# Kernel optimization log

Measured on AMD Instinct MI355X. Metric: run time of the kernel, lower is better.

The kernel has to match this reference:

```python
import jax, jax.numpy as jnp
import numpy as np

B, S, H = 1, 2048, 2048
HD, NQ, NKV = 128, 16, 4
FFH = 8192
EPS = 1e-5
ROPE_BASE = 10000.0
SOFTMAX_CAP = 50.0
CLIP_L, CLIP_R = 0.0, 1.0


def setup_inputs() -> dict:
    key = jax.random.key(0)
    ks = jax.random.split(key, 10)
    std = 0.02
    return {
        "x": jax.random.normal(ks[0], (B, S, H), dtype=jnp.float32),
        "attn_norm_w": jax.random.uniform(ks[1], (H,), minval=-1.0, maxval=1.0, dtype=jnp.float32),
        "mlp_norm_w": jax.random.uniform(ks[2], (H,), minval=-1.0, maxval=1.0, dtype=jnp.float32),
        "wq": jax.random.normal(ks[3], (H, NQ * HD), dtype=jnp.float32) * std,
        "wk": jax.random.normal(ks[4], (H, NKV * HD), dtype=jnp.float32) * std,
        "wv": jax.random.normal(ks[5], (H, NKV * HD), dtype=jnp.float32) * std,
        "wo": jax.random.normal(ks[6], (NQ * HD, H), dtype=jnp.float32) * std,
        "w_gate": jax.random.normal(ks[7], (H, FFH), dtype=jnp.float32) * std,
        "w_up": jax.random.normal(ks[8], (H, FFH), dtype=jnp.float32) * std,
        "w_down": jax.random.normal(ks[9], (FFH, H), dtype=jnp.float32) * std,
    }


def _rms_norm(x, w):
    # GroupRMSNorm with group_size=None -> whole hidden dim
    var = jnp.mean(jnp.square(x), axis=-1, keepdims=True)
    return x * jax.lax.rsqrt(var + EPS) * w


def _rope_cos_sin(seq_len, dim):
    inv_freq = 1.0 / (ROPE_BASE ** (jnp.arange(0, dim, 2, dtype=jnp.float32) / dim))
    t = jnp.arange(seq_len, dtype=jnp.float32)
    freqs = jnp.outer(t, inv_freq)                      # [S, dim/2]
    emb = jnp.concatenate([freqs, freqs], axis=-1)      # [S, dim]
    return jnp.cos(emb), jnp.sin(emb)


def _apply_rope(x, cos, sin):
    # x: [B, S, h, d]; rotate-half (LLaMA-style)
    d = x.shape[-1]
    x1, x2 = x[..., : d // 2], x[..., d // 2 :]
    rot = jnp.concatenate([-x2, x1], axis=-1)
    return x * cos[None, :, None, :] + rot * sin[None, :, None, :]


def _qk_norm(x):
    # per-head RMS norm over head_dim (qk_norm_group_size == head_dim), unit weight
    var = jnp.mean(jnp.square(x), axis=-1, keepdims=True)
    return x * jax.lax.rsqrt(var + EPS)


def reference(x, attn_norm_w, mlp_norm_w, wq, wk, wv, wo, w_gate, w_up, w_down):
    # ---- attention sub-layer ----
    h = _rms_norm(x, attn_norm_w)                                     # [B,S,H]
    q = (h @ wq).reshape(B, S, NQ, HD)
    k = (h @ wk).reshape(B, S, NKV, HD)
    v = (h @ wv).reshape(B, S, NKV, HD)

    cos, sin = _rope_cos_sin(S, HD)
    q = _apply_rope(q, cos, sin)
    k = _apply_rope(k, cos, sin)

    q = _qk_norm(q)
    k = _qk_norm(k)

    # GQA: expand kv heads to match q heads
    rep = NQ // NKV
    k = jnp.repeat(k, rep, axis=2)                                    # [B,S,NQ,HD]
    v = jnp.repeat(v, rep, axis=2)

    scale = 1.0 / jnp.sqrt(jnp.float32(HD))
    scores = jnp.einsum("bshd,bthd->bhst", q, k) * scale              # [B,NQ,S,S]
    # softmax cap: cap * tanh(s / cap)
    scores = SOFTMAX_CAP * jnp.tanh(scores / SOFTMAX_CAP)
    causal = jnp.tril(jnp.ones((S, S), dtype=bool))
    scores = jnp.where(causal[None, None], scores, -jnp.inf)
    p = jax.nn.softmax(scores, axis=-1)
    # clip range (l, r): clamp(p * (r - l) + l, 0, 1)
    p = jnp.clip(p * (CLIP_R - CLIP_L) + CLIP_L, 0.0, 1.0)
    o = jnp.einsum("bhst,bthd->bshd", p, v).reshape(B, S, NQ * HD)
    x = x + o @ wo

    # ---- MLP sub-layer (gated SiLU) ----
    h2 = _rms_norm(x, mlp_norm_w)
    mlp_out = (jax.nn.silu(h2 @ w_gate) * (h2 @ w_up)) @ w_down
    return x + mlp_out
```

## Files before the change

kernel.cpp:

```cpp
#include <hip/hip_runtime.h>

typedef __bf16 bf16;
typedef __bf16 bf16x8 __attribute__((ext_vector_type(8)));
typedef float f32x4 __attribute__((ext_vector_type(4)));

#define GLP16(gp, lp) __builtin_amdgcn_global_load_lds( \
    (const __attribute__((address_space(1))) void*)(gp), \
    (__attribute__((address_space(3))) void*)(lp), 16, 0, 0)

__device__ __forceinline__ f32x4 mfma16(bf16x8 a, bf16x8 b, f32x4 c) {
    return __builtin_amdgcn_mfma_f32_16x16x32_bf16(a, b, c, 0, 0, 0);
}

__global__ __launch_bounds__(256) void k_rmsnorm(const float* __restrict__ x,
        const float* __restrict__ w, bf16* __restrict__ out) {
    const int H = 2048;
    size_t row = blockIdx.x;
    const float* xr = x + row * H;
    int base = threadIdx.x * 8;
    float4 a = *(const float4*)(xr + base);
    float4 b = *(const float4*)(xr + base + 4);
    float ss = a.x*a.x + a.y*a.y + a.z*a.z + a.w*a.w
             + b.x*b.x + b.y*b.y + b.z*b.z + b.w*b.w;
#pragma unroll
    for (int m = 32; m > 0; m >>= 1) ss += __shfl_xor(ss, m);
    __shared__ float red[4];
    if ((threadIdx.x & 63) == 0) red[threadIdx.x >> 6] = ss;
    __syncthreads();
    float tot = red[0] + red[1] + red[2] + red[3];
    float rs = rsqrtf(tot * (1.0f / H) + 1e-5f);
    float4 wa = *(const float4*)(w + base);
    float4 wb = *(const float4*)(w + base + 4);
    bf16x8 ov;
    ov[0] = (bf16)(a.x * rs * wa.x); ov[1] = (bf16)(a.y * rs * wa.y);
    ov[2] = (bf16)(a.z * rs * wa.z); ov[3] = (bf16)(a.w * rs * wa.w);
    ov[4] = (bf16)(b.x * rs * wb.x); ov[5] = (bf16)(b.y * rs * wb.y);
    ov[6] = (bf16)(b.z * rs * wb.z); ov[7] = (bf16)(b.w * rs * wb.w);
    *(bf16x8*)(out + row * H + base) = ov;
}

__global__ __launch_bounds__(256) void k_convT(const float* __restrict__ W,
        bf16* __restrict__ Wt, int K, int N) {
    __shared__ float t[32][33];
    int k0 = blockIdx.x * 32, n0 = blockIdx.y * 32;
    int tx = threadIdx.x, ty = threadIdx.y;
#pragma unroll
    for (int i = 0; i < 4; i++)
        t[ty + i * 8][tx] = W[(size_t)(k0 + ty + i * 8) * N + n0 + tx];
    __syncthreads();
#pragma unroll
    for (int i = 0; i < 4; i++)
        Wt[(size_t)(n0 + ty + i * 8) * K + k0 + tx] = (bf16)t[tx][ty + i * 8];
}

__global__ __launch_bounds__(256) void k_transpose(const bf16* __restrict__ in,
        bf16* __restrict__ out, int R, int C) {
    __shared__ bf16 t[32][33];
    int r0 = blockIdx.x * 32, c0 = blockIdx.y * 32;
    int tx = threadIdx.x & 31, ty = threadIdx.x >> 5;
#pragma unroll
    for (int i = 0; i < 4; i++)
        t[ty + i * 8][tx] = in[(size_t)(r0 + ty + i * 8) * C + c0 + tx];
    __syncthreads();
#pragma unroll
    for (int i = 0; i < 4; i++)
        out[(size_t)(c0 + ty + i * 8) * R + r0 + tx] = t[tx][ty + i * 8];
}

template<int EPI>
__global__ __launch_bounds__(512) void k_gemm2(const bf16* __restrict__ A,
        const bf16* __restrict__ Bt, void* __restrict__ outp,
        const void* __restrict__ aux, int M, int N, int K, int ksplit) {
    extern __shared__ char lds[];
    const int tid = threadIdx.x, wave = tid >> 6, lane = tid & 63;
    const int lr = lane & 15, kg = lane >> 4;
    const int wm = wave >> 1, wn = wave & 1;
    const int bn = blockIdx.x, bm = blockIdx.y, split = blockIdx.z;
    const int row0 = bm * 256, col0 = bn * 128;
    const int kbeg = split * ksplit;
    const int NT = ksplit >> 6;
    const size_t K2 = (size_t)K * 2;

    size_t offA[4];
#pragma unroll
    for (int s = 0; s < 4; s++) {
        int d = s * 8192 + tid * 16;
        int ps = d ^ (((d >> 7) & 7) << 4);
        offA[s] = (size_t)(ps >> 7) * K2 + (ps & 127);
    }
    const char* Abase = (const char*)(A + (size_t)row0 * K + kbeg);
    const char* Bbase = (const char*)(Bt + (size_t)col0 * K + kbeg);

    auto stageA = [&](int t) {
        const char* src = Abase + (size_t)t * 128;
        char* dst = lds + ((t & 1) * 32768) + wave * 1024;
#pragma unroll
        for (int s = 0; s < 4; s++)
            GLP16(src + offA[s], dst + s * 8192);
    };
    auto stageB = [&](int t, int bidx) {
        const char* src = Bbase + (size_t)t * 128;
        char* dst = lds + 65536 + bidx * 16384 + wave * 1024;
#pragma unroll
        for (int s = 0; s < 2; s++)
            GLP16(src + offA[s], dst + s * 8192);
    };

    f32x4 acc[4][4];
#pragma unroll
    for (int m = 0; m < 4; m++)
#pragma unroll
        for (int n = 0; n < 4; n++) acc[m][n] = (f32x4){0, 0, 0, 0};

    stageA(0); stageB(0, 0); stageB(1, 1);
    asm volatile("s_waitcnt vmcnt(2)" ::: "memory");
    __builtin_amdgcn_s_barrier();
    __builtin_amdgcn_sched_barrier(0);
    asm volatile("" ::: "memory");

    const int xorm = (lr & 7) << 4;
    int bcur = 0;
    for (int t = 0; t < NT; ++t) {
        if (t + 1 < NT) stageA(t + 1);
        int bnx = bcur + 2; if (bnx >= 3) bnx -= 3;
        if (t + 2 < NT) stageB(t + 2, bnx);
        const char* As_ = lds + ((t & 1) * 32768);
        const char* Bs_ = lds + 65536 + bcur * 16384;
#pragma unroll
        for (int h = 0; h < 2; ++h) {
            const int inner = (h * 64 + kg * 16) ^ xorm;
            bf16x8 av[4], bv[4];
#pragma unroll
            for (int m = 0; m < 4; m++)
                av[m] = *(const bf16x8*)(As_ + (wm * 64 + m * 16 + lr) * 128 + inner);
#pragma unroll
            for (int n = 0; n < 4; n++)
                bv[n] = *(const bf16x8*)(Bs_ + (wn * 64 + n * 16 + lr) * 128 + inner);
#pragma unroll
            for (int m = 0; m < 4; m++)
#pragma unroll
                for (int n = 0; n < 4; n++)
                    acc[m][n] = mfma16(av[m], bv[n], acc[m][n]);
        }
        if (t + 1 < NT) {
            if (t + 2 < NT) asm volatile("s_waitcnt vmcnt(2)" ::: "memory");
            else            asm volatile("s_waitcnt vmcnt(0)" ::: "memory");
            __builtin_amdgcn_s_barrier();
            __builtin_amdgcn_sched_barrier(0);
            asm volatile("" ::: "memory");
        }
        bcur++; if (bcur == 3) bcur = 0;
    }

#pragma unroll
    for (int m = 0; m < 4; m++)
#pragma unroll
        for (int n = 0; n < 4; n++)
#pragma unroll
            for (int r = 0; r < 4; r++) {
                size_t row = row0 + wm * 64 + m * 16 + kg * 4 + r;
                size_t col = col0 + wn * 64 + n * 16 + lr;
                size_t idx = row * N + col;
                float vv = acc[m][n][r];
                if (EPI == 0) {
                    ((bf16*)outp)[idx] = (bf16)vv;
                } else if (EPI == 2) {
                    float g = (float)((const bf16*)aux)[idx];
                    float sg = g / (1.0f + __expf(-g));
                    ((bf16*)outp)[idx] = (bf16)(sg * vv);
                } else if (EPI == 3) {
                    ((float*)outp)[(size_t)split * M * N + idx] = vv;
                } else {
                    bf16* base = (bf16*)outp;
                    if (col < 2048)
                        base[row * 2048 + col] = (bf16)vv;
                    else if (col < 2560)
                        base[4194304 + row * 512 + (col - 2048)] = (bf16)vv;
                    else
                        base[5242880 + row * 512 + (col - 2560)] = (bf16)vv;
                }
            }
}

__global__ __launch_bounds__(256) void k_reduce(const float* __restrict__ parts,
        const float* __restrict__ resid, float* __restrict__ out,
        int ns, size_t n4) {
    size_t i = (size_t)blockIdx.x * 256 + threadIdx.x;
    if (i >= n4) return;
    float4 acc = ((const float4*)resid)[i];
    for (int s = 0; s < ns; s++) {
        float4 p = ((const float4*)(parts + (size_t)s * n4 * 4))[i];
        acc.x += p.x; acc.y += p.y; acc.z += p.z; acc.w += p.w;
    }
    ((float4*)out)[i] = acc;
}

__global__ __launch_bounds__(256) void k_reduce_rms(const float* __restrict__ parts,
        const float* __restrict__ resid, const float* __restrict__ w,
        float* __restrict__ x2, bf16* __restrict__ hb, int ns) {
    const int H = 2048;
    size_t row = blockIdx.x;
    int base = threadIdx.x * 8;
    const float* rr = resid + row * H + base;
    float4 a = *(const float4*)rr;
    float4 b = *(const float4*)(rr + 4);
    for (int s = 0; s < ns; s++) {
        const float* pp = parts + (size_t)s * H * 2048 + row * H + base;
        float4 pa = *(const float4*)pp;
        float4 pb = *(const float4*)(pp + 4);
        a.x += pa.x; a.y += pa.y; a.z += pa.z; a.w += pa.w;
        b.x += pb.x; b.y += pb.y; b.z += pb.z; b.w += pb.w;
    }
    *(float4*)(x2 + row * H + base) = a;
    *(float4*)(x2 + row * H + base + 4) = b;
    float ss = a.x*a.x + a.y*a.y + a.z*a.z + a.w*a.w
             + b.x*b.x + b.y*b.y + b.z*b.z + b.w*b.w;
#pragma unroll
    for (int m = 32; m > 0; m >>= 1) ss += __shfl_xor(ss, m);
    __shared__ float red[4];
    if ((threadIdx.x & 63) == 0) red[threadIdx.x >> 6] = ss;
    __syncthreads();
    float tot = red[0] + red[1] + red[2] + red[3];
    float rs = rsqrtf(tot * (1.0f / H) + 1e-5f);
    float4 wa = *(const float4*)(w + base);
    float4 wb = *(const float4*)(w + base + 4);
    bf16x8 ov;
    ov[0] = (bf16)(a.x * rs * wa.x); ov[1] = (bf16)(a.y * rs * wa.y);
    ov[2] = (bf16)(a.z * rs * wa.z); ov[3] = (bf16)(a.w * rs * wa.w);
    ov[4] = (bf16)(b.x * rs * wb.x); ov[5] = (bf16)(b.y * rs * wb.y);
    ov[6] = (bf16)(b.z * rs * wb.z); ov[7] = (bf16)(b.w * rs * wb.w);
    *(bf16x8*)(hb + row * H + base) = ov;
}

__global__ __launch_bounds__(64) void k_rope(bf16* __restrict__ q,
        bf16* __restrict__ k) {
    int s = blockIdx.x, hid = blockIdx.y, lane = threadIdx.x;
    bf16* p;
    if (hid < 16) p = q + (size_t)s * 2048 + hid * 128;
    else          p = k + (size_t)s * 512 + (hid - 16) * 128;
    float x1 = (float)p[lane], x2 = (float)p[lane + 64];
    float f = exp2f((float)lane * -0.2076205059304601f);
    float sn, cs;
    sincosf((float)s * f, &sn, &cs);
    float o1 = x1 * cs - x2 * sn;
    float o2 = x2 * cs + x1 * sn;
    float ss = o1 * o1 + o2 * o2;
#pragma unroll
    for (int m = 32; m > 0; m >>= 1) ss += __shfl_xor(ss, m);
    float rs = rsqrtf(ss * (1.0f / 128.0f) + 1e-5f);
    p[lane] = (bf16)(o1 * rs);
    p[lane + 64] = (bf16)(o2 * rs);
}

__global__ __launch_bounds__(256) void k_attn(const bf16* __restrict__ qg,
        const bf16* __restrict__ kgl, const bf16* __restrict__ vtg,
        bf16* __restrict__ og) {
    extern __shared__ char alds[];
    int pi = blockIdx.x, h = blockIdx.y, kvh = h >> 2;
    int tid = threadIdx.x, wave = tid >> 6, lane = tid & 63;
    int lr = lane & 15, kgrp = lane >> 4;

    int rowQ[4], colQ[4], rowV[4], colV[4];
#pragma unroll
    for (int j = 0; j < 4; j++) {
        int p = j * 4096 + wave * 1024 + lane * 16;
        int ps = p ^ (((p >> 8) & 7) << 4);
        rowQ[j] = ps >> 8; colQ[j] = ps & 255;
        int pv = p ^ (((p >> 7) & 7) << 4);
        rowV[j] = pv >> 7; colV[j] = pv & 127;
    }

    const float C1 = 0.08838834764831845f / 50.0f;
    const float L2E50 = 72.13475204444817f;

#pragma unroll 1
    for (int half = 0; half < 2; ++half) {
        int qt = half ? (31 - pi) : pi;
        int nt = qt + 1;

#pragma unroll
        for (int j = 0; j < 4; j++)
            GLP16((const char*)qg + (size_t)(qt * 64 + rowQ[j]) * 4096 + h * 256 + colQ[j],
                  alds + j * 4096 + wave * 1024);
        for (int t = 0; t < 2 && t < nt; t++) {
#pragma unroll
            for (int j = 0; j < 4; j++)
                GLP16((const char*)kgl + (size_t)(t * 64 + rowQ[j]) * 1024 + kvh * 256 + colQ[j],
                      alds + 16384 + t * 16384 + j * 4096 + wave * 1024);
#pragma unroll
            for (int j = 0; j < 4; j++)
                GLP16((const char*)vtg + (size_t)(kvh * 128 + rowV[j]) * 4096 + t * 128 + colV[j],
                      alds + 49152 + t * 16384 + j * 4096 + wave * 1024);
        }
        if (nt > 1) asm volatile("s_waitcnt vmcnt(8)" ::: "memory");
        else        asm volatile("s_waitcnt vmcnt(0)" ::: "memory");
        __builtin_amdgcn_s_barrier();

        bf16x8 qf[4];
#pragma unroll
        for (int c = 0; c < 4; c++) {
            int b = (wave * 16 + lr) * 256 + c * 64 + kgrp * 16;
            qf[c] = *(const bf16x8*)(alds + (b ^ (((b >> 8) & 7) << 4)));
        }
        f32x4 accO[8];
#pragma unroll
        for (int n = 0; n < 8; n++) accO[n] = (f32x4){0, 0, 0, 0};
        float lsum[4] = {0, 0, 0, 0};
        int qrow = qt * 64 + wave * 16 + kgrp * 4;

        for (int kt = 0; kt < nt; kt++) {
            int buf = kt & 1;
            const char* Kb = alds + 16384 + buf * 16384;
            const char* Vb = alds + 49152 + buf * 16384;
            char* Pb = alds + 81920;
#pragma unroll
            for (int j = 0; j < 4; j++) {
                f32x4 s = {0, 0, 0, 0};
#pragma unroll
                for (int c = 0; c < 4; c++) {
                    int b = (j * 16 + lr) * 256 + c * 64 + kgrp * 16;
                    bf16x8 kf = *(const bf16x8*)(Kb + (b ^ (((b >> 8) & 7) << 4)));
                    s = mfma16(qf[c], kf, s);
                }
                int key = kt * 64 + j * 16 + lr;
#pragma unroll
                for (int r = 0; r < 4; r++) {
                    float y = s[r] * C1;
                    float y2 = y * y;
                    float u = fmaf(y2, 0.13333333f, -0.33333333f);
                    u = fmaf(y2, u, 1.0f);
                    float t5 = y * u;
                    float pe = fmaf(t5, L2E50, -L2E50);
                    float pv = (key <= qrow + r) ? exp2f(pe) : 0.0f;
                    lsum[r] += pv;
                    int wb = (wave * 16 + kgrp * 4 + r) * 128 + (j * 16 + lr) * 2;
                    *(bf16*)(Pb + (wb ^ (((wb >> 7) & 7) << 4))) = (bf16)pv;
                }
            }
            bf16x8 pf[2];
#pragma unroll
            for (int ks2 = 0; ks2 < 2; ks2++) {
                int b = (wave * 16 + lr) * 128 + ks2 * 64 + kgrp * 16;
                pf[ks2] = *(const bf16x8*)(Pb + (b ^ (((b >> 7) & 7) << 4)));
            }
#pragma unroll
            for (int n = 0; n < 8; n++)
#pragma unroll
                for (int ks2 = 0; ks2 < 2; ks2++) {
                    int b = (n * 16 + lr) * 128 + ks2 * 64 + kgrp * 16;
                    bf16x8 vf = *(const bf16x8*)(Vb + (b ^ (((b >> 7) & 7) << 4)));
                    accO[n] = mfma16(pf[ks2], vf, accO[n]);
                }
            __builtin_amdgcn_s_barrier();
            bool more = (kt + 2 < nt);
            if (more) {
                int t = kt + 2;
#pragma unroll
                for (int j = 0; j < 4; j++)
                    GLP16((const char*)kgl + (size_t)(t * 64 + rowQ[j]) * 1024 + kvh * 256 + colQ[j],
                          alds + 16384 + buf * 16384 + j * 4096 + wave * 1024);
#pragma unroll
                for (int j = 0; j < 4; j++)
                    GLP16((const char*)vtg + (size_t)(kvh * 128 + rowV[j]) * 4096 + t * 128 + colV[j],
                          alds + 49152 + buf * 16384 + j * 4096 + wave * 1024);
            }
            if (kt + 1 < nt) {
                if (more) asm volatile("s_waitcnt vmcnt(8)" ::: "memory");
                else      asm volatile("s_waitcnt vmcnt(0)" ::: "memory");
                __builtin_amdgcn_s_barrier();
            }
        }
#pragma unroll
        for (int r = 0; r < 4; r++) {
            float t = lsum[r];
            t += __shfl_xor(t, 1); t += __shfl_xor(t, 2);
            t += __shfl_xor(t, 4); t += __shfl_xor(t, 8);
            lsum[r] = t;
        }
#pragma unroll
        for (int n = 0; n < 8; n++)
#pragma unroll
            for (int r = 0; r < 4; r++) {
                size_t row = qt * 64 + wave * 16 + kgrp * 4 + r;
                og[row * 2048 + h * 128 + n * 16 + lr] = (bf16)(accO[n][r] / lsum[r]);
            }
    }
}

extern "C" void kernel_launch(void* const* d_in, const int* in_sizes, int n_in,
                              void* d_out, int out_size, void* d_ws, size_t ws_size,
                              hipStream_t stream) {
    const float* x      = (const float*)d_in[0];
    const float* attn_w = (const float*)d_in[1];
    const float* mlp_w  = (const float*)d_in[2];
    const float* wq     = (const float*)d_in[3];
    const float* wk     = (const float*)d_in[4];
    const float* wv     = (const float*)d_in[5];
    const float* wo     = (const float*)d_in[6];
    const float* wgate  = (const float*)d_in[7];
    const float* wup    = (const float*)d_in[8];
    const float* wdown  = (const float*)d_in[9];
    float* out = (float*)d_out;
    char* ws = (char*)d_ws;

    const size_t MB = 1024 * 1024;
    bf16* W1  = (bf16*)(ws + 0);
    bf16* W2  = (bf16*)(ws + 32 * MB);
    bf16* W3  = (bf16*)(ws + 64 * MB);
    bf16* hb  = (bf16*)(ws + 96 * MB);
    bf16* qb  = (bf16*)(ws + 104 * MB);
    bf16* kb  = (bf16*)(ws + 112 * MB);
    bf16* vb  = (bf16*)(ws + 114 * MB);
    bf16* ob  = (bf16*)(ws + 116 * MB);
    float* x2 = (float*)(ws + 124 * MB);
    bf16* gb  = (bf16*)(ws + 140 * MB);
    bf16* vt  = (bf16*)(ws + 0);
    float* parts = (float*)(ws + 0);

    const int LDS2 = 114688;
    hipFuncSetAttribute((const void*)&k_gemm2<0>,
        hipFuncAttributeMaxDynamicSharedMemorySize, LDS2);
    hipFuncSetAttribute((const void*)&k_gemm2<2>,
        hipFuncAttributeMaxDynamicSharedMemorySize, LDS2);
    hipFuncSetAttribute((const void*)&k_gemm2<3>,
        hipFuncAttributeMaxDynamicSharedMemorySize, LDS2);
    hipFuncSetAttribute((const void*)&k_gemm2<4>,
        hipFuncAttributeMaxDynamicSharedMemorySize, LDS2);
    const int LDSA = 90112;
    hipFuncSetAttribute((const void*)&k_attn,
        hipFuncAttributeMaxDynamicSharedMemorySize, LDSA);

    dim3 cb(32, 8);
    const size_t n4 = (size_t)2048 * 2048 / 4;

    k_rmsnorm<<<2048, 256, 0, stream>>>(x, attn_w, hb);
    k_convT<<<dim3(64, 64), cb, 0, stream>>>(wq, W1, 2048, 2048);
    k_convT<<<dim3(64, 16), cb, 0, stream>>>(wk, W1 + 4194304, 2048, 512);
    k_convT<<<dim3(64, 16), cb, 0, stream>>>(wv, W1 + 5242880, 2048, 512);
    k_gemm2<4><<<dim3(24, 8, 1), 512, LDS2, stream>>>(hb, W1, qb, nullptr,
                                                      2048, 3072, 2048, 2048);
    k_transpose<<<dim3(64, 16), 256, 0, stream>>>(vb, vt, 2048, 512);
    k_rope<<<dim3(2048, 20), 64, 0, stream>>>(qb, kb);
    k_attn<<<dim3(16, 16), 256, LDSA, stream>>>(qb, kb, vt, ob);
    k_convT<<<dim3(64, 64), cb, 0, stream>>>(wo, W2, 2048, 2048);
    k_gemm2<3><<<dim3(16, 8, 2), 512, LDS2, stream>>>(ob, W2, parts, nullptr,
                                                      2048, 2048, 2048, 1024);
    k_reduce_rms<<<2048, 256, 0, stream>>>(parts, x, mlp_w, x2, hb, 2);
    k_convT<<<dim3(64, 256), cb, 0, stream>>>(wgate, W1, 2048, 8192);
    k_gemm2<0><<<dim3(64, 8, 1), 512, LDS2, stream>>>(hb, W1, gb, nullptr,
                                                      2048, 8192, 2048, 2048);
    k_convT<<<dim3(64, 256), cb, 0, stream>>>(wup, W2, 2048, 8192);
    k_gemm2<2><<<dim3(64, 8, 1), 512, LDS2, stream>>>(hb, W2, gb, gb,
                                                      2048, 8192, 2048, 2048);
    k_convT<<<dim3(256, 64), cb, 0, stream>>>(wdown, W3, 8192, 2048);
    k_gemm2<3><<<dim3(16, 8, 4), 512, LDS2, stream>>>(gb, W3, parts, nullptr,
                                                      2048, 2048, 8192, 2048);
    k_reduce<<<4096, 256, 0, stream>>>(parts, x2, out, 4, n4);
}
```

Measured before the change: 487.2 us.

## Replace GEMM with 256x256 tile kernel using 4-stage 32-wide K pipeline

```diff
diff --git a/kernel.cpp b/kernel.cpp
--- a/kernel.cpp
+++ b/kernel.cpp
@@ -1,6 +1,7 @@
 #include <hip/hip_runtime.h>
 
 typedef __bf16 bf16;
+typedef __bf16 bf16x4 __attribute__((ext_vector_type(4)));
 typedef __bf16 bf16x8 __attribute__((ext_vector_type(8)));
 typedef float f32x4 __attribute__((ext_vector_type(4)));
 
@@ -68,97 +69,107 @@
 }
 
 template<int EPI>
-__global__ __launch_bounds__(512) void k_gemm2(const bf16* __restrict__ A,
+__global__ __launch_bounds__(512, 2) void k_gemm3(const bf16* __restrict__ A,
         const bf16* __restrict__ Bt, void* __restrict__ outp,
         const void* __restrict__ aux, int M, int N, int K, int ksplit) {
     extern __shared__ char lds[];
     const int tid = threadIdx.x, wave = tid >> 6, lane = tid & 63;
     const int lr = lane & 15, kg = lane >> 4;
-    const int wm = wave >> 1, wn = wave & 1;
+    const int wm = wave >> 2, wn = wave & 3;
     const int bn = blockIdx.x, bm = blockIdx.y, split = blockIdx.z;
-    const int row0 = bm * 256, col0 = bn * 128;
+    const int row0 = bm * 256, col0 = bn * 256;
     const int kbeg = split * ksplit;
-    const int NT = ksplit >> 6;
+    const int NT = ksplit >> 5;
     const size_t K2 = (size_t)K * 2;
 
-    size_t offA[4];
-#pragma unroll
-    for (int s = 0; s < 4; s++) {
+    size_t offS[2];
+#pragma unroll
+    for (int s = 0; s < 2; s++) {
         int d = s * 8192 + tid * 16;
-        int ps = d ^ (((d >> 7) & 7) << 4);
-        offA[s] = (size_t)(ps >> 7) * K2 + (ps & 127);
-    }
-    const char* Abase = (const char*)(A + (size_t)row0 * K + kbeg);
-    const char* Bbase = (const char*)(Bt + (size_t)col0 * K + kbeg);
-
-    auto stageA = [&](int t) {
-        const char* src = Abase + (size_t)t * 128;
-        char* dst = lds + ((t & 1) * 32768) + wave * 1024;
-#pragma unroll
-        for (int s = 0; s < 4; s++)
-            GLP16(src + offA[s], dst + s * 8192);
+        int line = d >> 7, w = d & 127;
+        int w2 = w ^ ((line & 7) << 4);
+        offS[s] = (size_t)(line * 2 + (w2 >> 6)) * K2 + (w2 & 63);
+    }
+    const char* Ab = (const char*)A + ((size_t)row0 * K + kbeg) * 2;
+    const char* Bb = (const char*)Bt + ((size_t)col0 * K + kbeg) * 2;
+
+    auto stA = [&](int s) {
+        const char* src = Ab + (size_t)s * 64;
+        char* dst = lds + (s & 3) * 16384 + wave * 1024;
+        GLP16(src + offS[0], dst);
+        GLP16(src + offS[1], dst + 8192);
     };
-    auto stageB = [&](int t, int bidx) {
-        const char* src = Bbase + (size_t)t * 128;
-        char* dst = lds + 65536 + bidx * 16384 + wave * 1024;
-#pragma unroll
-        for (int s = 0; s < 2; s++)
-            GLP16(src + offA[s], dst + s * 8192);
+    auto stB = [&](int s) {
+        const char* src = Bb + (size_t)s * 64;
+        char* dst = lds + 65536 + (s & 3) * 16384 + wave * 1024;
+        GLP16(src + offS[0], dst);
+        GLP16(src + offS[1], dst + 8192);
     };
-
-    f32x4 acc[4][4];
-#pragma unroll
-    for (int m = 0; m < 4; m++)
+    auto frag = [&](const char* base, int row) -> bf16x8 {
+        int line = row >> 1;
+        int pos = (((row & 1) << 6) + (kg << 4)) ^ ((line & 7) << 4);
+        return *(const bf16x8*)(base + line * 128 + pos);
+    };
+
+    f32x4 acc[8][4];
+#pragma unroll
+    for (int m = 0; m < 8; m++)
 #pragma unroll
         for (int n = 0; n < 4; n++) acc[m][n] = (f32x4){0, 0, 0, 0};
 
-    stageA(0); stageB(0, 0); stageB(1, 1);
-    asm volatile("s_waitcnt vmcnt(2)" ::: "memory");
+    stA(0); stB(0);
+    if (NT > 1) { stA(1); stB(1); }
+    if (NT > 2) { stA(2); stB(2); }
+    if (NT > 2)      asm volatile("s_waitcnt vmcnt(8)" ::: "memory");
+    else if (NT > 1) asm volatile("s_waitcnt vmcnt(4)" ::: "memory");
+    else             asm volatile("s_waitcnt vmcnt(0)" ::: "memory");
     __builtin_amdgcn_s_barrier();
-    __builtin_amdgcn_sched_barrier(0);
-    asm volatile("" ::: "memory");
-
-    const int xorm = (lr & 7) << 4;
-    int bcur = 0;
-    for (int t = 0; t < NT; ++t) {
-        if (t + 1 < NT) stageA(t + 1);
-        int bnx = bcur + 2; if (bnx >= 3) bnx -= 3;
-        if (t + 2 < NT) stageB(t + 2, bnx);
-        const char* As_ = lds + ((t & 1) * 32768);
-        const char* Bs_ = lds + 65536 + bcur * 16384;
-#pragma unroll
-        for (int h = 0; h < 2; ++h) {
-            const int inner = (h * 64 + kg * 16) ^ xorm;
-            bf16x8 av[4], bv[4];
-#pragma unroll
-            for (int m = 0; m < 4; m++)
-                av[m] = *(const bf16x8*)(As_ + (wm * 64 + m * 16 + lr) * 128 + inner);
+
+    for (int s = 0; s < NT; ++s) {
+        const char* As_ = lds + (s & 3) * 16384;
+        const char* Bs_ = lds + 65536 + (s & 3) * 16384;
+        bf16x8 av[4], bv[4];
+#pragma unroll
+        for (int m = 0; m < 4; m++) av[m] = frag(As_, wm * 128 + m * 16 + lr);
+#pragma unroll
+        for (int n = 0; n < 4; n++) bv[n] = frag(Bs_, wn * 64 + n * 16 + lr);
+        if (s + 3 < NT) stA(s + 3);
+        __builtin_amdgcn_s_barrier();
+        asm volatile("s_waitcnt lgkmcnt(0)" ::: "memory");
+        __builtin_amdgcn_s_setprio(1);
+#pragma unroll
+        for (int m = 0; m < 4; m++)
 #pragma unroll
             for (int n = 0; n < 4; n++)
-                bv[n] = *(const bf16x8*)(Bs_ + (wn * 64 + n * 16 + lr) * 128 + inner);
-#pragma unroll
-            for (int m = 0; m < 4; m++)
-#pragma unroll
-                for (int n = 0; n < 4; n++)
-                    acc[m][n] = mfma16(av[m], bv[n], acc[m][n]);
-        }
-        if (t + 1 < NT) {
-            if (t + 2 < NT) asm volatile("s_waitcnt vmcnt(2)" ::: "memory");
-            else            asm volatile("s_waitcnt vmcnt(0)" ::: "memory");
-            __builtin_amdgcn_s_barrier();
-            __builtin_amdgcn_sched_barrier(0);
-            asm volatile("" ::: "memory");
-        }
-        bcur++; if (bcur == 3) bcur = 0;
-    }
-
-#pragma unroll
-    for (int m = 0; m < 4; m++)
+                acc[m][n] = mfma16(av[m], bv[n], acc[m][n]);
+        __builtin_amdgcn_s_setprio(0);
+        __builtin_amdgcn_s_barrier();
+        bf16x8 aw[4];
+#pragma unroll
+        for (int m = 0; m < 4; m++) aw[m] = frag(As_, wm * 128 + (m + 4) * 16 + lr);
+        if (s + 3 < NT) stB(s + 3);
+        __builtin_amdgcn_s_barrier();
+        asm volatile("s_waitcnt lgkmcnt(0)" ::: "memory");
+        __builtin_amdgcn_s_setprio(1);
+#pragma unroll
+        for (int m = 0; m < 4; m++)
+#pragma unroll
+            for (int n = 0; n < 4; n++)
+                acc[m + 4][n] = mfma16(aw[m], bv[n], acc[m + 4][n]);
+        __builtin_amdgcn_s_setprio(0);
+        if (s + 3 < NT)      asm volatile("s_waitcnt vmcnt(8)" ::: "memory");
+        else if (s + 2 < NT) asm volatile("s_waitcnt vmcnt(4)" ::: "memory");
+        else if (s + 1 < NT) asm volatile("s_waitcnt vmcnt(0)" ::: "memory");
+        __builtin_amdgcn_s_barrier();
+    }
+
+#pragma unroll
+    for (int m = 0; m < 8; m++)
 #pragma unroll
         for (int n = 0; n < 4; n++)
 #pragma unroll
             for (int r = 0; r < 4; r++) {
-                size_t row = row0 + wm * 64 + m * 16 + kg * 4 + r;
+                size_t row = row0 + wm * 128 + m * 16 + kg * 4 + r;
                 size_t col = col0 + wn * 64 + n * 16 + lr;
                 size_t idx = row * N + col;
                 float vv = acc[m][n][r];
@@ -168,16 +179,8 @@
                     float g = (float)((const bf16*)aux)[idx];
                     float sg = g / (1.0f + __expf(-g));
                     ((bf16*)outp)[idx] = (bf16)(sg * vv);
-                } else if (EPI == 3) {
+                } else {
                     ((float*)outp)[(size_t)split * M * N + idx] = vv;
-                } else {
-                    bf16* base = (bf16*)outp;
-                    if (col < 2048)
-                        base[row * 2048 + col] = (bf16)vv;
-                    else if (col < 2560)
-                        base[4194304 + row * 512 + (col - 2048)] = (bf16)vv;
-                    else
-                        base[5242880 + row * 512 + (col - 2560)] = (bf16)vv;
                 }
             }
 }
@@ -232,6 +235,22 @@
     *(bf16x8*)(hb + row * H + base) = ov;
 }
 
+__global__ __launch_bounds__(256) void k_qkvfin(const float* __restrict__ parts,
+        bf16* __restrict__ qb, bf16* __restrict__ kb, bf16* __restrict__ vb) {
+    int s = blockIdx.x;
+    int col = blockIdx.y * 1024 + threadIdx.x * 4;
+    const float* p0 = parts + (size_t)s * 3072 + col;
+    const float* p1 = p0 + (size_t)2048 * 3072;
+    float4 a = *(const float4*)p0;
+    float4 b = *(const float4*)p1;
+    a.x += b.x; a.y += b.y; a.z += b.z; a.w += b.w;
+    bf16x4 o;
+    o[0] = (bf16)a.x; o[1] = (bf16)a.y; o[2] = (bf16)a.z; o[3] = (bf16)a.w;
+    if (col < 2048)      *(bf16x4*)(qb + (size_t)s * 2048 + col) = o;
+    else if (col < 2560) *(bf16x4*)(kb + (size_t)s * 512 + col - 2048) = o;
+    else                 *(bf16x4*)(vb + (size_t)s * 512 + col - 2560) = o;
+}
+
 __global__ __launch_bounds__(64) void k_rope(bf16* __restrict__ q,
         bf16* __restrict__ k) {
     int s = blockIdx.x, hid = blockIdx.y, lane = threadIdx.x;
@@ -416,16 +435,15 @@
     bf16* gb  = (bf16*)(ws + 140 * MB);
     bf16* vt  = (bf16*)(ws + 0);
     float* parts = (float*)(ws + 0);
-
-    const int LDS2 = 114688;
-    hipFuncSetAttribute((const void*)&k_gemm2<0>,
-        hipFuncAttributeMaxDynamicSharedMemorySize, LDS2);
-    hipFuncSetAttribute((const void*)&k_gemm2<2>,
-        hipFuncAttributeMaxDynamicSharedMemorySize, LDS2);
-    hipFuncSetAttribute((const void*)&k_gemm2<3>,
-        hipFuncAttributeMaxDynamicSharedMemorySize, LDS2);
-    hipFuncSetAttribute((const void*)&k_gemm2<4>,
-        hipFuncAttributeMaxDynamicSharedMemorySize, LDS2);
+    float* partsq = (float*)(ws + 116 * MB);
+
+    const int LDS3 = 131072;
+    hipFuncSetAttribute((const void*)&k_gemm3<0>,
+        hipFuncAttributeMaxDynamicSharedMemorySize, LDS3);
+    hipFuncSetAttribute((const void*)&k_gemm3<2>,
+        hipFuncAttributeMaxDynamicSharedMemorySize, LDS3);
+    hipFuncSetAttribute((const void*)&k_gemm3<3>,
+        hipFuncAttributeMaxDynamicSharedMemorySize, LDS3);
     const int LDSA = 90112;
     hipFuncSetAttribute((const void*)&k_attn,
         hipFuncAttributeMaxDynamicSharedMemorySize, LDSA);
@@ -437,23 +455,24 @@
     k_convT<<<dim3(64, 64), cb, 0, stream>>>(wq, W1, 2048, 2048);
     k_convT<<<dim3(64, 16), cb, 0, stream>>>(wk, W1 + 4194304, 2048, 512);
     k_convT<<<dim3(64, 16), cb, 0, stream>>>(wv, W1 + 5242880, 2048, 512);
-    k_gemm2<4><<<dim3(24, 8, 1), 512, LDS2, stream>>>(hb, W1, qb, nullptr,
-                                                      2048, 3072, 2048, 2048);
+    k_gemm3<3><<<dim3(12, 8, 2), 512, LDS3, stream>>>(hb, W1, partsq, nullptr,
+                                                      2048, 3072, 2048, 1024);
+    k_qkvfin<<<dim3(2048, 3), 256, 0, stream>>>(partsq, qb, kb, vb);
     k_transpose<<<dim3(64, 16), 256, 0, stream>>>(vb, vt, 2048, 512);
     k_rope<<<dim3(2048, 20), 64, 0, stream>>>(qb, kb);
     k_attn<<<dim3(16, 16), 256, LDSA, stream>>>(qb, kb, vt, ob);
     k_convT<<<dim3(64, 64), cb, 0, stream>>>(wo, W2, 2048, 2048);
-    k_gemm2<3><<<dim3(16, 8, 2), 512, LDS2, stream>>>(ob, W2, parts, nullptr,
-                                                      2048, 2048, 2048, 1024);
+    k_gemm3<3><<<dim3(8, 8, 2), 512, LDS3, stream>>>(ob, W2, parts, nullptr,
+                                                     2048, 2048, 2048, 1024);
     k_reduce_rms<<<2048, 256, 0, stream>>>(parts, x, mlp_w, x2, hb, 2);
     k_convT<<<dim3(64, 256), cb, 0, stream>>>(wgate, W1, 2048, 8192);
-    k_gemm2<0><<<dim3(64, 8, 1), 512, LDS2, stream>>>(hb, W1, gb, nullptr,
+    k_gemm3<0><<<dim3(32, 8, 1), 512, LDS3, stream>>>(hb, W1, gb, nullptr,
                                                       2048, 8192, 2048, 2048);
     k_convT<<<dim3(64, 256), cb, 0, stream>>>(wup, W2, 2048, 8192);
-    k_gemm2<2><<<dim3(64, 8, 1), 512, LDS2, stream>>>(hb, W2, gb, gb,
+    k_gemm3<2><<<dim3(32, 8, 1), 512, LDS3, stream>>>(hb, W2, gb, gb,
                                                       2048, 8192, 2048, 2048);
     k_convT<<<dim3(256, 64), cb, 0, stream>>>(wdown, W3, 8192, 2048);
-    k_gemm2<3><<<dim3(16, 8, 4), 512, LDS2, stream>>>(gb, W3, parts, nullptr,
-                                                      2048, 2048, 8192, 2048);
+    k_gemm3<3><<<dim3(8, 8, 4), 512, LDS3, stream>>>(gb, W3, parts, nullptr,
+                                                     2048, 2048, 8192, 2048);
     k_reduce<<<4096, 256, 0, stream>>>(parts, x2, out, 4, n4);
 }
```

Result: no change. 489.7 us (+0.5%).
